# Kernel tuning notes

Measured on AMD Instinct MI355X. Metric: run time of the kernel, lower is better.

Reference implementation:

```python
import jax, jax.numpy as jnp
import numpy as np

N_HIDDENS = 8
RESCALE_RATE = 8  # max_duration // n_hiddens = 64 // 8


def setup_inputs() -> dict:
    key = jax.random.key(0)
    k1, k2, k3, k4, k5 = jax.random.split(key, 5)
    T, B, I, H, N = 256, 64, 256, 256, N_HIDDENS
    k = float(np.sqrt(1.0 / H))
    return {
        "x": jax.random.normal(k1, (T, B, I), dtype=jnp.float32),
        "fix_duration": jax.random.randint(k2, (T, B), 0, 64, dtype=jnp.int32),
        "weight": jax.random.uniform(k3, (N, I + H, 4 * H), dtype=jnp.float32, minval=-k, maxval=k),
        "bias_i": jax.random.uniform(k4, (N, 4 * H), dtype=jnp.float32, minval=-k, maxval=k),
        "bias_h": jax.random.uniform(k5, (N, 4 * H), dtype=jnp.float32, minval=-k, maxval=k),
    }


def reference(x, fix_duration, weight, bias_i, bias_h):
    # x: [T, B, I]; fix_duration: [T, B] int; weight: [N, I+H, 4H]; biases: [N, 4H]
    T, B, I = x.shape
    N, _, F4 = weight.shape
    H = F4 // 4
    bias = (bias_i + bias_h)[:, None, :]          # [N, 1, 4H]
    branch_idx = jnp.arange(N)[:, None]           # [N, 1]

    def step(carry, inp):
        h, c = carry                               # each [N, B, H]
        xt, dur = inp                              # [B, I], [B] int
        # mask: 1.0 for branches that freeze their cell state this step
        mask = (branch_idx > (dur // RESCALE_RATE)[None, :]).astype(h.dtype)[:, :, None]  # [N, B, 1]
        xN = jnp.broadcast_to(xt[None], (N, B, I))
        combined = jnp.concatenate([xN, h], axis=2)                 # [N, B, I+H]
        z = jnp.einsum('nbd,ndf->nbf', combined, weight) + bias     # [N, B, 4H]
        i_g = jax.nn.sigmoid(z[..., :H])
        f_g = jax.nn.sigmoid(z[..., H:2 * H])
        o_g = jax.nn.sigmoid(z[..., 2 * H:3 * H])
        g = jnp.tanh(z[..., 3 * H:])
        c_new = f_g * c + i_g * g
        c_new = c_new * (1.0 - mask) + c * mask                     # blend with old cell state
        h_new = o_g * jnp.tanh(c_new)
        return (h_new, c_new), h_new

    h0 = jnp.zeros((N, B, H), dtype=x.dtype)
    c0 = jnp.zeros((N, B, H), dtype=x.dtype)
    (_, _), hs = jax.lax.scan(step, (h0, c0), (x, fix_duration))
    return hs  # [T, N, B, H]
```

## Files before the change

kernel.cpp:

```cpp
#include <hip/hip_runtime.h>
#include <hip/hip_bf16.h>

#define T_STEPS 256
#define BATCH   64
#define DIM_I   256
#define DIM_H   256
#define NBR     8
#define F_DIM   1024

typedef __attribute__((ext_vector_type(8))) short short8;
typedef __attribute__((ext_vector_type(4))) float floatx4;

#define WX_OFF  0u
#define WH_OFF  (4u<<20)
#define C_OFF   (8u<<20)
#define H_OFF   ((8u<<20) + 0x80000u)
#define ZX_OFF  (16u<<20)

__device__ __forceinline__ float sigmoid_fast(float x) {
    return 1.0f / (1.0f + __expf(-x));
}
__device__ __forceinline__ float tanh_fast(float x) {
    return 1.0f - 2.0f / (__expf(2.0f * x) + 1.0f);
}
__device__ __forceinline__ short f2bf(float f) {
    unsigned u = __float_as_uint(f);
    u += 0x7FFFu + ((u >> 16) & 1u);
    return (short)(u >> 16);
}

__global__ void __launch_bounds__(256)
prep_kernel(const float* __restrict__ weight, short* __restrict__ wx,
            short* __restrict__ wh) {
    int id = blockIdx.x * 256 + threadIdx.x;
    int f  = id & 1023;
    int kk = (id >> 10) & 511;
    int n  = id >> 19;
    float v = weight[(size_t)id];
    int ks = (kk & 255) >> 5;
    int qr = (kk >> 3) & 3;
    int j  = kk & 7;
    int ct = f >> 4;
    int c0 = f & 15;
    int lane = qr * 16 + c0;
    size_t o = ((((size_t)n * 8 + ks) * 64 + ct) * 64 + lane) * 8 + j;
    (kk < 256 ? wx : wh)[o] = f2bf(v);
}

__global__ void __launch_bounds__(256)
xgemm_kernel(const float* __restrict__ x, const short* __restrict__ wxg,
             const float* __restrict__ bias_i, const float* __restrict__ bias_h,
             floatx4* __restrict__ zx, int t0) {
    const int tid = threadIdx.x;
    const int lane = tid & 63, w = tid >> 6;
    const int l15 = lane & 15, quad = lane >> 4;
    const int n = blockIdx.x & 7;
    const int tt = blockIdx.x >> 3;
    const int t = t0 + tt;

    const short8* wx8 = (const short8*)wxg + (size_t)n * 8 * 64 * 64;

    short8 a[4][8];
#pragma unroll
    for (int m = 0; m < 4; ++m) {
        const float* xr = x + ((size_t)t * BATCH + m * 16 + l15) * DIM_I + quad * 8;
#pragma unroll
        for (int ks = 0; ks < 8; ++ks) {
            const floatx4* p = (const floatx4*)(xr + ks * 32);
            floatx4 u = p[0], v = p[1];
            short8 af;
            af[0] = f2bf(u[0]); af[1] = f2bf(u[1]); af[2] = f2bf(u[2]); af[3] = f2bf(u[3]);
            af[4] = f2bf(v[0]); af[5] = f2bf(v[1]); af[6] = f2bf(v[2]); af[7] = f2bf(v[3]);
            a[m][ks] = af;
        }
    }

    for (int ci = 0; ci < 16; ++ci) {
        const int ct = w * 16 + ci;
        float bb = bias_i[n * F_DIM + ct * 16 + l15] + bias_h[n * F_DIM + ct * 16 + l15];
        short8 bw[8];
#pragma unroll
        for (int ks = 0; ks < 8; ++ks)
            bw[ks] = wx8[(ks * 64 + ct) * 64 + lane];
#pragma unroll
        for (int m = 0; m < 4; ++m) {
            floatx4 acc = (floatx4){bb, bb, bb, bb};
#pragma unroll
            for (int ks = 0; ks < 8; ++ks)
                acc = __builtin_amdgcn_mfma_f32_16x16x32_bf16(a[m][ks], bw[ks], acc, 0, 0, 0);
            zx[((((size_t)tt * 8 + n) * 4 + m) * 64 + ct) * 64 + lane] = acc;
        }
    }
}

__global__ void __launch_bounds__(512, 2)
rec_kernel(const floatx4* __restrict__ zx, const int* __restrict__ dur,
           const short* __restrict__ whg, float* __restrict__ out,
           float* __restrict__ c_carry, short* __restrict__ h_carry,
           int t0, int CT) {
    __shared__ short hlds[2][16 * 264];

    const int tid = threadIdx.x;
    const int lane = tid & 63, w = tid >> 6;
    const int l15 = lane & 15, quad = lane >> 4;
    const int n = blockIdx.x & 7;
    const int rt = blockIdx.x >> 3;
    const int r0 = rt * 16;

    const short8* wh8 = (const short8*)whg + (size_t)n * 8 * 64 * 64;

    {
        const short8* src = (const short8*)(h_carry + ((size_t)n * 4 + rt) * 4096);
        int row = tid >> 5, cg = tid & 31;
        *(short8*)((char*)&hlds[0][0] + row * 528 + cg * 16) = src[tid];
    }
    float c[2][4];
    {
        const float* cp = c_carry + (((size_t)n * 4 + rt) * 512 + tid) * 8;
#pragma unroll
        for (int q = 0; q < 2; ++q)
#pragma unroll
            for (int r = 0; r < 4; ++r) c[q][r] = cp[q * 4 + r];
    }
    short8 wr0[8], wr1[8];
#pragma unroll
    for (int ci = 0; ci < 8; ++ci) {
        const int ct = (ci >> 1) * 16 + w * 2 + (ci & 1);
        wr0[ci] = wh8[(0 * 64 + ct) * 64 + lane];
        wr1[ci] = wh8[(1 * 64 + ct) * 64 + lane];
    }
    floatx4 pf[8];
#pragma unroll
    for (int ci = 0; ci < 8; ++ci) {
        const int ct = (ci >> 1) * 16 + w * 2 + (ci & 1);
        pf[ci] = zx[(((size_t)0 * 8 + n) * 4 + rt) * 4096 + ct * 64 + lane];
    }
    __syncthreads();

    for (int tt = 0; tt < CT; ++tt) {
        const int t = t0 + tt;
        char* hc = (char*)&hlds[tt & 1][0];
        char* hn = (char*)&hlds[(tt + 1) & 1][0];

        short8 a[8];
#pragma unroll
        for (int ks = 0; ks < 8; ++ks)
            a[ks] = *(const short8*)(hc + l15 * 528 + ks * 64 + quad * 16);

        floatx4 acc[8];
#pragma unroll
        for (int ci = 0; ci < 8; ++ci) acc[ci] = pf[ci];

        int d4[4];
#pragma unroll
        for (int r = 0; r < 4; ++r)
            d4[r] = dur[(size_t)t * BATCH + r0 + quad * 4 + r];

        {
            const int ttn = (tt + 1 < CT) ? tt + 1 : tt;
#pragma unroll
            for (int ci = 0; ci < 8; ++ci) {
                const int ct = (ci >> 1) * 16 + w * 2 + (ci & 1);
                pf[ci] = zx[(((size_t)ttn * 8 + n) * 4 + rt) * 4096 + ct * 64 + lane];
            }
        }

        short8 sb[2][6];
#pragma unroll
        for (int ks = 0; ks < 6; ++ks)
            sb[0][ks] = wh8[((ks + 2) * 64 + (w * 2)) * 64 + lane];

#pragma unroll
        for (int ci = 0; ci < 8; ++ci) {
            if (ci < 7) {
                const int ctn = ((ci + 1) >> 1) * 16 + w * 2 + ((ci + 1) & 1);
#pragma unroll
                for (int ks = 0; ks < 6; ++ks)
                    sb[(ci + 1) & 1][ks] = wh8[((ks + 2) * 64 + ctn) * 64 + lane];
            }
            acc[ci] = __builtin_amdgcn_mfma_f32_16x16x32_bf16(a[0], wr0[ci], acc[ci], 0, 0, 0);
            acc[ci] = __builtin_amdgcn_mfma_f32_16x16x32_bf16(a[1], wr1[ci], acc[ci], 0, 0, 0);
#pragma unroll
            for (int ks = 0; ks < 6; ++ks)
                acc[ci] = __builtin_amdgcn_mfma_f32_16x16x32_bf16(a[ks + 2], sb[ci & 1][ks], acc[ci], 0, 0, 0);
        }

#pragma unroll
        for (int r = 0; r < 4; ++r) {
            const bool freeze = n > (d4[r] >> 3);
            const int row = quad * 4 + r;
#pragma unroll
            for (int q = 0; q < 2; ++q) {
                float zi = acc[0 + q][r];
                float zf = acc[2 + q][r];
                float zo = acc[4 + q][r];
                float zg = acc[6 + q][r];
                float ig = sigmoid_fast(zi);
                float fg = sigmoid_fast(zf);
                float og = sigmoid_fast(zo);
                float gg = tanh_fast(zg);
                float cn = freeze ? c[q][r] : fg * c[q][r] + ig * gg;
                c[q][r] = cn;
                float hv = og * tanh_fast(cn);
                const int hcol = w * 32 + q * 16 + l15;
                out[(((size_t)t * NBR + n) * BATCH + (r0 + row)) * DIM_H + hcol] = hv;
                *(short*)(hn + row * 528 + hcol * 2) = f2bf(hv);
            }
        }
        __syncthreads();
    }

    {
        float* cp = c_carry + (((size_t)n * 4 + rt) * 512 + tid) * 8;
#pragma unroll
        for (int q = 0; q < 2; ++q)
#pragma unroll
            for (int r = 0; r < 4; ++r) cp[q * 4 + r] = c[q][r];
        char* hf = (char*)&hlds[CT & 1][0];
        short8* dst = (short8*)(h_carry + ((size_t)n * 4 + rt) * 4096);
        int row = tid >> 5, cg = tid & 31;
        dst[tid] = *(const short8*)(hf + row * 528 + cg * 16);
    }
}

extern "C" void kernel_launch(void* const* d_in, const int* in_sizes, int n_in,
                              void* d_out, int out_size, void* d_ws, size_t ws_size,
                              hipStream_t stream) {
    const float* x      = (const float*)d_in[0];
    const int*   durp   = (const int*)d_in[1];
    const float* weight = (const float*)d_in[2];
    const float* bias_i = (const float*)d_in[3];
    const float* bias_h = (const float*)d_in[4];
    float* out = (float*)d_out;
    char*  ws  = (char*)d_ws;

    short*   wx      = (short*)(ws + WX_OFF);
    short*   wh      = (short*)(ws + WH_OFF);
    float*   c_carry = (float*)(ws + C_OFF);
    short*   h_carry = (short*)(ws + H_OFF);
    floatx4* zxp     = (floatx4*)(ws + ZX_OFF);

    int CT = 256;
    while (CT > 2 && (size_t)ZX_OFF + (size_t)CT * 2097152ull > ws_size) CT >>= 1;

    hipMemsetAsync(ws + C_OFF, 0, 524288 + 262144, stream);

    prep_kernel<<<16384, 256, 0, stream>>>(weight, wx, wh);

    for (int t0 = 0; t0 < T_STEPS; t0 += CT) {
        xgemm_kernel<<<CT * 8, 256, 0, stream>>>(x, wx, bias_i, bias_h, zxp, t0);
        rec_kernel<<<32, 512, 0, stream>>>(zxp, durp, wh, out, c_carry, h_carry, t0, CT);
    }
}
```

Measured before the change: 2.844 ms.

## Keep recurrent weights resident in registers and swizzle hidden-state LDS

Loads all eight k-slices of the per-wave recurrent weight fragments into registers once, instead of streaming six slices from global memory on every timestep. Replaces the padded LDS hidden-state layout with an XOR swizzle, and unrolls the time loop by two with ping-pong prefetch buffers for zx and vectorized duration loads. The aim is to take global weight loads off the serial recurrence's critical path, at the cost of much higher register pressure and a risk of spills.

```diff
diff --git a/kernel.cpp b/kernel.cpp
--- a/kernel.cpp
+++ b/kernel.cpp
@@ -98,7 +98,7 @@
            const short* __restrict__ whg, float* __restrict__ out,
            float* __restrict__ c_carry, short* __restrict__ h_carry,
            int t0, int CT) {
-    __shared__ short hlds[2][16 * 264];
+    __shared__ short hlds[2][16 * 256];
 
     const int tid = threadIdx.x;
     const int lane = tid & 63, w = tid >> 6;
@@ -108,11 +108,14 @@
     const int r0 = rt * 16;
 
     const short8* wh8 = (const short8*)whg + (size_t)n * 8 * 64 * 64;
+    const int swz = (l15 & 7) << 4;
+    char* h0 = (char*)&hlds[0][0];
+    char* h1 = (char*)&hlds[1][0];
 
     {
         const short8* src = (const short8*)(h_carry + ((size_t)n * 4 + rt) * 4096);
         int row = tid >> 5, cg = tid & 31;
-        *(short8*)((char*)&hlds[0][0] + row * 528 + cg * 16) = src[tid];
+        *(short8*)(h0 + row * 512 + ((cg * 16) ^ ((row & 7) << 4))) = src[tid];
     }
     float c[2][4];
     {
@@ -122,93 +125,85 @@
 #pragma unroll
             for (int r = 0; r < 4; ++r) c[q][r] = cp[q * 4 + r];
     }
-    short8 wr0[8], wr1[8];
+    short8 wr[8][8];
+#pragma unroll
+    for (int ks = 0; ks < 8; ++ks)
+#pragma unroll
+        for (int ci = 0; ci < 8; ++ci) {
+            const int ct = (ci >> 1) * 16 + w * 2 + (ci & 1);
+            wr[ks][ci] = wh8[(ks * 64 + ct) * 64 + lane];
+        }
+
+    const size_t zxb = (size_t)(n * 4 + rt) * 4096 + lane;
+    floatx4 pfA[8], pfB[8];
+    int4 dA, dB;
 #pragma unroll
     for (int ci = 0; ci < 8; ++ci) {
         const int ct = (ci >> 1) * 16 + w * 2 + (ci & 1);
-        wr0[ci] = wh8[(0 * 64 + ct) * 64 + lane];
-        wr1[ci] = wh8[(1 * 64 + ct) * 64 + lane];
-    }
-    floatx4 pf[8];
-#pragma unroll
-    for (int ci = 0; ci < 8; ++ci) {
-        const int ct = (ci >> 1) * 16 + w * 2 + (ci & 1);
-        pf[ci] = zx[(((size_t)0 * 8 + n) * 4 + rt) * 4096 + ct * 64 + lane];
-    }
+        pfA[ci] = zx[zxb + ct * 64];
+    }
+    dA = *(const int4*)(dur + (size_t)t0 * BATCH + r0 + quad * 4);
+
     __syncthreads();
 
-    for (int tt = 0; tt < CT; ++tt) {
-        const int t = t0 + tt;
-        char* hc = (char*)&hlds[tt & 1][0];
-        char* hn = (char*)&hlds[(tt + 1) & 1][0];
-
-        short8 a[8];
-#pragma unroll
-        for (int ks = 0; ks < 8; ++ks)
-            a[ks] = *(const short8*)(hc + l15 * 528 + ks * 64 + quad * 16);
-
-        floatx4 acc[8];
-#pragma unroll
-        for (int ci = 0; ci < 8; ++ci) acc[ci] = pf[ci];
-
-        int d4[4];
-#pragma unroll
-        for (int r = 0; r < 4; ++r)
-            d4[r] = dur[(size_t)t * BATCH + r0 + quad * 4 + r];
-
-        {
-            const int ttn = (tt + 1 < CT) ? tt + 1 : tt;
-#pragma unroll
-            for (int ci = 0; ci < 8; ++ci) {
-                const int ct = (ci >> 1) * 16 + w * 2 + (ci & 1);
-                pf[ci] = zx[(((size_t)ttn * 8 + n) * 4 + rt) * 4096 + ct * 64 + lane];
-            }
-        }
-
-        short8 sb[2][6];
-#pragma unroll
-        for (int ks = 0; ks < 6; ++ks)
-            sb[0][ks] = wh8[((ks + 2) * 64 + (w * 2)) * 64 + lane];
-
-#pragma unroll
-        for (int ci = 0; ci < 8; ++ci) {
-            if (ci < 7) {
-                const int ctn = ((ci + 1) >> 1) * 16 + w * 2 + ((ci + 1) & 1);
-#pragma unroll
-                for (int ks = 0; ks < 6; ++ks)
-                    sb[(ci + 1) & 1][ks] = wh8[((ks + 2) * 64 + ctn) * 64 + lane];
-            }
-            acc[ci] = __builtin_amdgcn_mfma_f32_16x16x32_bf16(a[0], wr0[ci], acc[ci], 0, 0, 0);
-            acc[ci] = __builtin_amdgcn_mfma_f32_16x16x32_bf16(a[1], wr1[ci], acc[ci], 0, 0, 0);
-#pragma unroll
-            for (int ks = 0; ks < 6; ++ks)
-                acc[ci] = __builtin_amdgcn_mfma_f32_16x16x32_bf16(a[ks + 2], sb[ci & 1][ks], acc[ci], 0, 0, 0);
-        }
-
-#pragma unroll
-        for (int r = 0; r < 4; ++r) {
-            const bool freeze = n > (d4[r] >> 3);
-            const int row = quad * 4 + r;
-#pragma unroll
-            for (int q = 0; q < 2; ++q) {
-                float zi = acc[0 + q][r];
-                float zf = acc[2 + q][r];
-                float zo = acc[4 + q][r];
-                float zg = acc[6 + q][r];
-                float ig = sigmoid_fast(zi);
-                float fg = sigmoid_fast(zf);
-                float og = sigmoid_fast(zo);
-                float gg = tanh_fast(zg);
-                float cn = freeze ? c[q][r] : fg * c[q][r] + ig * gg;
-                c[q][r] = cn;
-                float hv = og * tanh_fast(cn);
-                const int hcol = w * 32 + q * 16 + l15;
-                out[(((size_t)t * NBR + n) * BATCH + (r0 + row)) * DIM_H + hcol] = hv;
-                *(short*)(hn + row * 528 + hcol * 2) = f2bf(hv);
-            }
-        }
+#define STEP(TT, HC, HN, PFC, PFN, DC, DN)                                     \
+    {                                                                          \
+        const int t_ = t0 + (TT);                                              \
+          \
+        short8 a_[8];                                                          \
+        _Pragma("unroll")                                                      \
+        for (int ks = 0; ks < 8; ++ks)                                         \
+            a_[ks] = *(const short8*)((HC) + l15 * 512 +                       \
+                                      ((ks * 64 + quad * 16) ^ swz));          \
+            \
+        const int ttn_ = ((TT) + 1 < CT) ? (TT) + 1 : (TT);                    \
+        _Pragma("unroll")                                                      \
+        for (int ci = 0; ci < 8; ++ci) {                                       \
+            const int ct_ = (ci >> 1) * 16 + w * 2 + (ci & 1);                 \
+            (PFN)[ci] = zx[(size_t)ttn_ * 131072 + zxb + ct_ * 64];            \
+        }                                                                      \
+        (DN) = *(const int4*)(dur + (size_t)(t0 + ttn_) * BATCH + r0 + quad * 4); \
+                         \
+        _Pragma("unroll")                                                      \
+        for (int ci = 0; ci < 8; ++ci) {                                       \
+            _Pragma("unroll")                                                  \
+            for (int ks = 0; ks < 8; ++ks)                                     \
+                (PFC)[ci] = __builtin_amdgcn_mfma_f32_16x16x32_bf16(           \
+                    a_[ks], wr[ks][ci], (PFC)[ci], 0, 0, 0);                   \
+        }                                                                      \
+                                      \
+        const int dv_[4] = {(DC).x, (DC).y, (DC).z, (DC).w};                   \
+        _Pragma("unroll")                                                      \
+        for (int r = 0; r < 4; ++r) {                                          \
+            const bool freeze = n > (dv_[r] >> 3);                             \
+            const int row = quad * 4 + r;                                      \
+            _Pragma("unroll")                                                  \
+            for (int q = 0; q < 2; ++q) {                                      \
+                float zi = (PFC)[0 + q][r];                                    \
+                float zf = (PFC)[2 + q][r];                                    \
+                float zo = (PFC)[4 + q][r];                                    \
+                float zg = (PFC)[6 + q][r];                                    \
+                float ig = sigmoid_fast(zi);                                   \
+                float fg = sigmoid_fast(zf);                                   \
+                float og = sigmoid_fast(zo);                                   \
+                float gg = tanh_fast(zg);                                      \
+                float cn = freeze ? c[q][r] : fg * c[q][r] + ig * gg;          \
+                c[q][r] = cn;                                                  \
+                float hv = og * tanh_fast(cn);                                 \
+                const int hcol = w * 32 + q * 16 + l15;                        \
+                out[(((size_t)t_ * NBR + n) * BATCH + (r0 + row)) * DIM_H + hcol] = hv; \
+                *(short*)((HN) + row * 512 + ((2 * hcol) ^ ((row & 7) << 4))) = f2bf(hv); \
+            }                                                                  \
+        }                                                                      \
+    }
+
+    for (int tt = 0; tt < CT; tt += 2) {
+        STEP(tt,     h0, h1, pfA, pfB, dA, dB);
         __syncthreads();
-    }
+        STEP(tt + 1, h1, h0, pfB, pfA, dB, dA);
+        __syncthreads();
+    }
+#undef STEP
 
     {
         float* cp = c_carry + (((size_t)n * 4 + rt) * 512 + tid) * 8;
@@ -216,10 +211,9 @@
         for (int q = 0; q < 2; ++q)
 #pragma unroll
             for (int r = 0; r < 4; ++r) cp[q * 4 + r] = c[q][r];
-        char* hf = (char*)&hlds[CT & 1][0];
-        short8* dst = (short8*)(h_carry + ((size_t)n * 4 + rt) * 4096);
         int row = tid >> 5, cg = tid & 31;
-        dst[tid] = *(const short8*)(hf + row * 528 + cg * 16);
+        short8 v = *(const short8*)(h0 + row * 512 + ((cg * 16) ^ ((row & 7) << 4)));
+        ((short8*)(h_carry + ((size_t)n * 4 + rt) * 4096))[tid] = v;
     }
 }
 
```

New measurement: 3.396 ms. +19.4%, slower.
